# Optimization experiments

Hardware: AMD Instinct MI355X
Metric: run time of the kernel (lower is better)

The kernel has to match this reference:

```python
import jax, jax.numpy as jnp
import numpy as np

N_EMBD = 1024
N_HEAD = 16
B, T = 2, 2048
LN_EPS = 1e-5


def _linear_params(key, d_in, d_out):
    k1, k2 = jax.random.split(key)
    bound = 1.0 / np.sqrt(d_in)
    W = jax.random.uniform(k1, (d_in, d_out), jnp.float32, -bound, bound)
    b = jax.random.uniform(k2, (d_out,), jnp.float32, -bound, bound)
    return W, b


def setup_inputs() -> dict:
    key = jax.random.key(0)
    ks = jax.random.split(key, 8)
    x = jax.random.normal(ks[0], (B, T, N_EMBD), jnp.float32)
    Wq, bq = _linear_params(ks[1], N_EMBD, N_EMBD)
    Wk, bk = _linear_params(ks[2], N_EMBD, N_EMBD)
    Wv, bv = _linear_params(ks[3], N_EMBD, N_EMBD)
    Wo, bo = _linear_params(ks[4], N_EMBD, N_EMBD)
    W1, b1 = _linear_params(ks[5], N_EMBD, 4 * N_EMBD)
    W2, b2 = _linear_params(ks[6], 4 * N_EMBD, N_EMBD)
    ln1_g = jnp.ones((N_EMBD,), jnp.float32)
    ln1_b = jnp.zeros((N_EMBD,), jnp.float32)
    ln2_g = jnp.ones((N_EMBD,), jnp.float32)
    ln2_b = jnp.zeros((N_EMBD,), jnp.float32)
    return dict(x=x, Wq=Wq, bq=bq, Wk=Wk, bk=bk, Wv=Wv, bv=bv, Wo=Wo, bo=bo,
                W1=W1, b1=b1, W2=W2, b2=b2,
                ln1_g=ln1_g, ln1_b=ln1_b, ln2_g=ln2_g, ln2_b=ln2_b)


def _layernorm(x, g, b):
    mu = jnp.mean(x, axis=-1, keepdims=True)
    var = jnp.mean(jnp.square(x - mu), axis=-1, keepdims=True)
    return (x - mu) * jax.lax.rsqrt(var + LN_EPS) * g + b


def _attention(x, Wq, bq, Wk, bk, Wv, bv, Wo, bo):
    Bsz, Tlen, C = x.shape
    hd = C // N_HEAD
    q = (x @ Wq + bq).reshape(Bsz, Tlen, N_HEAD, hd)
    k = (x @ Wk + bk).reshape(Bsz, Tlen, N_HEAD, hd)
    v = (x @ Wv + bv).reshape(Bsz, Tlen, N_HEAD, hd)
    scale = 1.0 / np.sqrt(hd)
    # NOTE: the original module's mask buffer is all ones -> masked_fill is a
    # no-op, so attention is FULL (non-causal) despite the class name.
    att = jnp.einsum('bqhd,bkhd->bhqk', q, k) * scale
    att = jax.nn.softmax(att, axis=-1)
    y = jnp.einsum('bhqk,bkhd->bqhd', att, v).reshape(Bsz, Tlen, C)
    return y @ Wo + bo


def reference(x, Wq, bq, Wk, bk, Wv, bv, Wo, bo, W1, b1, W2, b2,
              ln1_g, ln1_b, ln2_g, ln2_b):
    x = x + _attention(_layernorm(x, ln1_g, ln1_b), Wq, bq, Wk, bk, Wv, bv, Wo, bo)
    h = _layernorm(x, ln2_g, ln2_b)
    h = jax.nn.gelu(h @ W1 + b1, approximate=False) @ W2 + b2
    return x + h
```

## Files before the change

### kernel.cpp

```cpp
#include <hip/hip_runtime.h>
#include <hip/hip_bf16.h>
#include <math.h>


typedef __bf16 bf16x8 __attribute__((ext_vector_type(8)));
typedef float f32x4 __attribute__((ext_vector_type(4)));

__device__ __forceinline__ unsigned short f2bf(float f) {
  union { float f; unsigned int u; } v; v.f = f;
  unsigned int u = v.u;
  unsigned int r = (u + 0x7fffu + ((u >> 16) & 1u)) >> 16;
  return (unsigned short)r;
}

__device__ __forceinline__ unsigned int fbits(float f) {
  union { float f; unsigned int u; } v; v.f = f;
  return v.u;
}

__device__ __forceinline__ bf16x8 ld_bf16x8(const unsigned short* p) {
  union { uint4 u; bf16x8 v; } x;
  x.u = *(const uint4*)p;
  return x.v;
}

__device__ __forceinline__ float fast_exp2(float x) {
#if __has_builtin(__builtin_amdgcn_exp2f)
  return __builtin_amdgcn_exp2f(x);
#else
  return exp2f(x);
#endif
}

__device__ __forceinline__ void barrier_lgkm_only() {
  asm volatile("s_waitcnt lgkmcnt(0)\n\ts_barrier" ::: "memory");
}

__device__ __forceinline__ void async_copy16(const void* g, void* l) {
  __builtin_amdgcn_global_load_lds(
      (const __attribute__((address_space(1))) void*)g,
      (__attribute__((address_space(3))) void*)l, 16, 0, 0);
}

__global__ __launch_bounds__(256) void transpose_cast_kernel(
    const float* __restrict__ W, unsigned short* __restrict__ Wt, int N, int K) {
  __shared__ unsigned short tile[32][33];
  const int n0 = blockIdx.x * 32, k0 = blockIdx.y * 32;
  const int t = threadIdx.x;
  const int r = t >> 3, cq = (t & 7) * 4;
  float4 v = *(const float4*)&W[(size_t)(k0 + r) * N + n0 + cq];
  tile[cq + 0][r] = f2bf(v.x);
  tile[cq + 1][r] = f2bf(v.y);
  tile[cq + 2][r] = f2bf(v.z);
  tile[cq + 3][r] = f2bf(v.w);
  __syncthreads();
  ushort4 o;
  o.x = tile[r][cq + 0];
  o.y = tile[r][cq + 1];
  o.z = tile[r][cq + 2];
  o.w = tile[r][cq + 3];
  *(ushort4*)&Wt[(size_t)(n0 + r) * K + k0 + cq] = o;
}

__global__ __launch_bounds__(256) void transpose_v_kernel(
    const unsigned short* __restrict__ V, unsigned short* __restrict__ Vt) {
  __shared__ unsigned short tile[32][36];
  const int kt = blockIdx.x * 32;
  const int d0 = blockIdx.y * 32;
  const int bh = blockIdx.z;
  const int bb = bh >> 4, h = bh & 15;
  const int t = threadIdx.x;
  const int r = t >> 3, c4 = (t & 7) * 4;
  ushort4 v = *(const ushort4*)&V[((size_t)bb * 2048 + kt + r) * 1024 + h * 64 + d0 + c4];
  tile[c4 + 0][r] = v.x;
  tile[c4 + 1][r] = v.y;
  tile[c4 + 2][r] = v.z;
  tile[c4 + 3][r] = v.w;
  __syncthreads();
  ushort4 o;
  o.x = tile[r][c4 + 0];
  o.y = tile[r][c4 + 1];
  o.z = tile[r][c4 + 2];
  o.w = tile[r][c4 + 3];
  *(ushort4*)&Vt[((size_t)bh * 64 + d0 + r) * 2048 + kt + c4] = o;
}

__global__ __launch_bounds__(256) void ln_kernel(
    const float* __restrict__ x, const float* __restrict__ g,
    const float* __restrict__ b, unsigned short* __restrict__ out) {
  const int row = blockIdx.x, t = threadIdx.x;
  const float4 v = ((const float4*)(x + (size_t)row * 1024))[t];
  float s = v.x + v.y + v.z + v.w;
  float s2 = v.x * v.x + v.y * v.y + v.z * v.z + v.w * v.w;
  for (int o = 32; o > 0; o >>= 1) {
    s += __shfl_xor(s, o, 64);
    s2 += __shfl_xor(s2, o, 64);
  }
  __shared__ float red[8];
  const int w = t >> 6;
  if ((t & 63) == 0) { red[w] = s; red[4 + w] = s2; }
  __syncthreads();
  s = red[0] + red[1] + red[2] + red[3];
  s2 = red[4] + red[5] + red[6] + red[7];
  const float mu = s * (1.f / 1024.f);
  const float var = s2 * (1.f / 1024.f) - mu * mu;
  const float rs = rsqrtf(var + 1e-5f);
  const float4 gg = ((const float4*)g)[t];
  const float4 bb = ((const float4*)b)[t];
  ushort4 o4;
  o4.x = f2bf((v.x - mu) * rs * gg.x + bb.x);
  o4.y = f2bf((v.y - mu) * rs * gg.y + bb.y);
  o4.z = f2bf((v.z - mu) * rs * gg.z + bb.z);
  o4.w = f2bf((v.w - mu) * rs * gg.w + bb.w);
  ((ushort4*)(out + (size_t)row * 1024))[t] = o4;
}

enum { MODE_QKV = 0, MODE_RES = 1, MODE_GELU = 2 };

#define QSCALE 0.18033688011112043f

template <int BM, int BN, int MODE>
__global__ __launch_bounds__(256) void gemm_kernel(
    const unsigned short* __restrict__ A, const unsigned short* __restrict__ Bt,
    const float* __restrict__ bias0, const float* __restrict__ bias1,
    const float* __restrict__ bias2, const float* __restrict__ residual,
    void* __restrict__ out0, void* __restrict__ out1, void* __restrict__ out2,
    int M, int N, int K) {
  constexpr int MI = BM / 32;
  constexpr int NI = BN / 32;
  __shared__ __align__(16) unsigned short As[2][2][BM * 32];
  __shared__ __align__(16) unsigned short Bs[2][2][BN * 32];
  const int t = threadIdx.x;

  const int NT = N / BN;
  const int NTX = NT >> 3;
  const int bid = blockIdx.x;
  const int xcd = bid & 7, local = bid >> 3;
  const int nt_ = xcd * NTX + local % NTX;
  const int mt = local / NTX;
  const int m0 = mt * BM, n0 = nt_ * BN;

  const int l = t & 63, w = t >> 6;
  const int wm = (w >> 1) * (BM / 2), wn = (w & 1) * (BN / 2);
  const int lr = l & 15, lq = l >> 4;

  f32x4 acc[MI][NI];
#pragma unroll
  for (int i = 0; i < MI; i++)
#pragma unroll
    for (int j = 0; j < NI; j++) {
      f32x4 z = {0.f, 0.f, 0.f, 0.f};
      acc[i][j] = z;
    }

  auto issue = [&](int k0, int p) {
#pragma unroll
    for (int h = 0; h < 2; h++)
#pragma unroll
      for (int s = 0; s < BM / 64; s++) {
        const int c = t + s * 256;
        const int row = c >> 2, k8 = (c & 3) * 8;
        async_copy16(&A[(size_t)(m0 + row) * K + k0 + h * 32 + k8],
                     &As[p][h][c * 8]);
      }
#pragma unroll
    for (int h = 0; h < 2; h++)
#pragma unroll
      for (int s = 0; s < BN / 64; s++) {
        const int c = t + s * 256;
        const int row = c >> 2, k8 = (c & 3) * 8;
        async_copy16(&Bt[(size_t)(n0 + row) * K + k0 + h * 32 + k8],
                     &Bs[p][h][c * 8]);
      }
  };

  issue(0, 0);
  int p = 0;
  for (int k0 = 0; k0 < K; k0 += 64) {
    __syncthreads();
    if (k0 + 64 < K) issue(k0 + 64, p ^ 1);
#pragma unroll
    for (int kk = 0; kk < 2; kk++) {
      bf16x8 af[MI], bf[NI];
#pragma unroll
      for (int mi = 0; mi < MI; mi++)
        af[mi] = ld_bf16x8(&As[p][kk][(wm + mi * 16 + lr) * 32 + lq * 8]);
#pragma unroll
      for (int ni = 0; ni < NI; ni++)
        bf[ni] = ld_bf16x8(&Bs[p][kk][(wn + ni * 16 + lr) * 32 + lq * 8]);
#pragma unroll
      for (int mi = 0; mi < MI; mi++)
#pragma unroll
        for (int ni = 0; ni < NI; ni++)
          acc[mi][ni] = __builtin_amdgcn_mfma_f32_16x16x32_bf16(
              af[mi], bf[ni], acc[mi][ni], 0, 0, 0);
    }
    p ^= 1;
  }

#pragma unroll
  for (int mi = 0; mi < MI; mi++) {
#pragma unroll
    for (int ni = 0; ni < NI; ni++) {
#pragma unroll
      for (int i = 0; i < 4; i++) {
        const int gm = m0 + wm + mi * 16 + lq * 4 + i;
        const int gn = n0 + wn + ni * 16 + lr;
        const float v = acc[mi][ni][i];
        if (MODE == MODE_QKV) {
          const int sel = gn >> 10, cn = gn & 1023;
          const float* bb = sel == 0 ? bias0 : (sel == 1 ? bias1 : bias2);
          unsigned short* dst =
              (unsigned short*)(sel == 0 ? out0 : (sel == 1 ? out1 : out2));
          float u = v + bb[cn];
          if (sel == 0) u *= QSCALE;
          dst[(size_t)gm * 1024 + cn] = f2bf(u);
        } else if (MODE == MODE_RES) {
          ((float*)out0)[(size_t)gm * N + gn] =
              v + bias0[gn] + residual[(size_t)gm * N + gn];
        } else {
          const float u = v + bias0[gn];
          const float ge = 0.5f * u * (1.f + erff(u * 0.70710678118654752f));
          ((unsigned short*)out0)[(size_t)gm * N + gn] = f2bf(ge);
        }
      }
    }
  }
}

__global__ __launch_bounds__(256) void attn_kernel(
    const unsigned short* __restrict__ Q, const unsigned short* __restrict__ Kt,
    const unsigned short* __restrict__ Vt, unsigned short* __restrict__ O) {
  __shared__ __align__(16) unsigned short QPs[128 * 72];
  __shared__ __align__(16) unsigned short Ks[2][64 * 72];
  __shared__ __align__(16) unsigned short Vs[2][64 * 72];
  const int id = blockIdx.x;
  const int xcd = id & 7, loc = id >> 3;
  const int bh = xcd * 4 + (loc >> 4);
  const int qt = loc & 15;
  const int bb = bh >> 4, h = bh & 15;
  const int t = threadIdx.x, l = t & 63, w = t >> 6;
  const int lr = l & 15, lq = l >> 4;
  const size_t rowBase = (size_t)bb * 2048;
  const int col0 = h * 64;

  const int sr = t >> 3;
  const int sc8 = (t & 7) * 8;

  uint4 kreg[2], vreg[2];
  auto issue_kv = [&](int kt) {
#pragma unroll
    for (int s = 0; s < 2; s++) {
      const int r = sr + s * 32;
      kreg[s] = *(const uint4*)&Kt[(rowBase + kt + r) * 1024 + col0 + sc8];
      vreg[s] = *(const uint4*)&Vt[((size_t)bh * 64 + r) * 2048 + kt + sc8];
    }
  };
  auto write_kv = [&](int p) {
#pragma unroll
    for (int s = 0; s < 2; s++) {
      const int r = sr + s * 32;
      *(uint4*)&Ks[p][r * 72 + sc8] = kreg[s];
      *(uint4*)&Vs[p][r * 72 + sc8] = vreg[s];
    }
  };

  issue_kv(0);

#pragma unroll
  for (int s = 0; s < 4; s++) {
    const int c = t + s * 256;
    const int r = c >> 3, c8 = (c & 7) * 8;
    *(uint4*)&QPs[r * 72 + c8] =
        *(const uint4*)&Q[(rowBase + qt * 128 + r) * 1024 + col0 + c8];
  }
  barrier_lgkm_only();
  bf16x8 qf[2][2];
#pragma unroll
  for (int s = 0; s < 2; s++)
#pragma unroll
    for (int kk = 0; kk < 2; kk++)
      qf[s][kk] = ld_bf16x8(&QPs[(w * 32 + s * 16 + lr) * 72 + kk * 32 + lq * 8]);

  write_kv(0);
  issue_kv(64);
  barrier_lgkm_only();

  f32x4 oacc[2][4];
#pragma unroll
  for (int s = 0; s < 2; s++)
#pragma unroll
    for (int nt = 0; nt < 4; nt++) {
      f32x4 z = {0.f, 0.f, 0.f, 0.f};
      oacc[s][nt] = z;
    }
  float lp[2] = {0.f, 0.f};

  int p = 0;
  for (int kt = 0; kt < 2048; kt += 64) {
    if (kt + 64 < 2048) {
      write_kv(p ^ 1);
      if (kt + 128 < 2048) issue_kv(kt + 128);
    }

    f32x4 st[2][4];
#pragma unroll
    for (int s = 0; s < 2; s++)
#pragma unroll
      for (int nt = 0; nt < 4; nt++) {
        f32x4 z = {0.f, 0.f, 0.f, 0.f};
        st[s][nt] = z;
      }
#pragma unroll
    for (int nt = 0; nt < 4; nt++) {
      bf16x8 kf0 = ld_bf16x8(&Ks[p][(nt * 16 + lr) * 72 + 0 * 32 + lq * 8]);
      bf16x8 kf1 = ld_bf16x8(&Ks[p][(nt * 16 + lr) * 72 + 1 * 32 + lq * 8]);
      __builtin_amdgcn_s_setprio(1);
      st[0][nt] = __builtin_amdgcn_mfma_f32_16x16x32_bf16(kf0, qf[0][0], st[0][nt], 0, 0, 0);
      st[1][nt] = __builtin_amdgcn_mfma_f32_16x16x32_bf16(kf0, qf[1][0], st[1][nt], 0, 0, 0);
      st[0][nt] = __builtin_amdgcn_mfma_f32_16x16x32_bf16(kf1, qf[0][1], st[0][nt], 0, 0, 0);
      st[1][nt] = __builtin_amdgcn_mfma_f32_16x16x32_bf16(kf1, qf[1][1], st[1][nt], 0, 0, 0);
      __builtin_amdgcn_s_setprio(0);
    }

    bf16x8 vf[2][4];
#pragma unroll
    for (int kb = 0; kb < 2; kb++)
#pragma unroll
      for (int nt = 0; nt < 4; nt++)
        vf[kb][nt] = ld_bf16x8(&Vs[p][(nt * 16 + lr) * 72 + kb * 32 + lq * 8]);

#pragma unroll
    for (int s = 0; s < 2; s++) {
      float rsum = 0.f;
#pragma unroll
      for (int nt = 0; nt < 4; nt++)
#pragma unroll
        for (int i = 0; i < 4; i++) {
          const float pv = fast_exp2(st[s][nt][i]);
          st[s][nt][i] = pv;
          rsum += pv;
        }
      lp[s] += rsum;
    }

#pragma unroll
    for (int s = 0; s < 2; s++)
#pragma unroll
      for (int nt = 0; nt < 4; nt++) {
        uint2 pk;
        pk.x = __builtin_amdgcn_perm(fbits(st[s][nt][1]), fbits(st[s][nt][0]), 0x07060302u);
        pk.y = __builtin_amdgcn_perm(fbits(st[s][nt][3]), fbits(st[s][nt][2]), 0x07060302u);
        *(uint2*)&QPs[(w * 32 + s * 16 + lr) * 72 + nt * 16 + lq * 4] = pk;
      }

#pragma unroll
    for (int kb = 0; kb < 2; kb++) {
      bf16x8 pf0 = ld_bf16x8(&QPs[(w * 32 + lr) * 72 + kb * 32 + lq * 8]);
      bf16x8 pf1 = ld_bf16x8(&QPs[(w * 32 + 16 + lr) * 72 + kb * 32 + lq * 8]);
      __builtin_amdgcn_s_setprio(1);
#pragma unroll
      for (int nt = 0; nt < 4; nt++) {
        oacc[0][nt] = __builtin_amdgcn_mfma_f32_16x16x32_bf16(pf0, vf[kb][nt], oacc[0][nt], 0, 0, 0);
        oacc[1][nt] = __builtin_amdgcn_mfma_f32_16x16x32_bf16(pf1, vf[kb][nt], oacc[1][nt], 0, 0, 0);
      }
      __builtin_amdgcn_s_setprio(0);
    }

    if (kt + 64 < 2048) barrier_lgkm_only();
    p ^= 1;
  }

#pragma unroll
  for (int s = 0; s < 2; s++) {
    float li = lp[s];
    li += __shfl_xor(li, 16, 64);
    li += __shfl_xor(li, 32, 64);
    const float inv = 1.f / li;
#pragma unroll
    for (int nt = 0; nt < 4; nt++)
#pragma unroll
      for (int i = 0; i < 4; i++) {
        const size_t orow = rowBase + qt * 128 + w * 32 + s * 16 + lq * 4 + i;
        const int ocol = col0 + nt * 16 + lr;
        O[orow * 1024 + ocol] = f2bf(oacc[s][nt][i] * inv);
      }
  }
}

extern "C" void kernel_launch(void* const* d_in, const int* in_sizes, int n_in,
                              void* d_out, int out_size, void* d_ws, size_t ws_size,
                              hipStream_t stream) {
  const float* x    = (const float*)d_in[0];
  const float* Wq   = (const float*)d_in[1];
  const float* bq   = (const float*)d_in[2];
  const float* Wk   = (const float*)d_in[3];
  const float* bk   = (const float*)d_in[4];
  const float* Wv   = (const float*)d_in[5];
  const float* bv   = (const float*)d_in[6];
  const float* Wo   = (const float*)d_in[7];
  const float* bo   = (const float*)d_in[8];
  const float* W1   = (const float*)d_in[9];
  const float* b1   = (const float*)d_in[10];
  const float* W2   = (const float*)d_in[11];
  const float* b2   = (const float*)d_in[12];
  const float* ln1g = (const float*)d_in[13];
  const float* ln1b = (const float*)d_in[14];
  const float* ln2g = (const float*)d_in[15];
  const float* ln2b = (const float*)d_in[16];

  char* ws = (char*)d_ws;
  const size_t MB = 1024ull * 1024ull;
  unsigned short* WqT = (unsigned short*)(ws + 0 * MB);
  unsigned short* WkT = (unsigned short*)(ws + 2 * MB);
  unsigned short* WvT = (unsigned short*)(ws + 4 * MB);
  unsigned short* WoT = (unsigned short*)(ws + 6 * MB);
  unsigned short* W1T = (unsigned short*)(ws + 8 * MB);
  unsigned short* W2T = (unsigned short*)(ws + 16 * MB);
  unsigned short* xn  = (unsigned short*)(ws + 24 * MB);
  unsigned short* Qb  = (unsigned short*)(ws + 32 * MB);
  unsigned short* Kb  = (unsigned short*)(ws + 40 * MB);
  unsigned short* Vb  = (unsigned short*)(ws + 48 * MB);
  unsigned short* Ob  = (unsigned short*)(ws + 56 * MB);
  float*          x1  = (float*)(ws + 64 * MB);
  unsigned short* h2  = (unsigned short*)(ws + 80 * MB);
  unsigned short* VtG = (unsigned short*)(ws + 24 * MB);
  unsigned short* Hb  = (unsigned short*)(ws + 24 * MB);

  const dim3 blk(256);

  transpose_cast_kernel<<<dim3(32, 32), blk, 0, stream>>>(Wq, WqT, 1024, 1024);
  transpose_cast_kernel<<<dim3(32, 32), blk, 0, stream>>>(Wk, WkT, 1024, 1024);
  transpose_cast_kernel<<<dim3(32, 32), blk, 0, stream>>>(Wv, WvT, 1024, 1024);
  transpose_cast_kernel<<<dim3(32, 32), blk, 0, stream>>>(Wo, WoT, 1024, 1024);
  transpose_cast_kernel<<<dim3(128, 32), blk, 0, stream>>>(W1, W1T, 4096, 1024);
  transpose_cast_kernel<<<dim3(32, 128), blk, 0, stream>>>(W2, W2T, 1024, 4096);

  ln_kernel<<<4096, blk, 0, stream>>>(x, ln1g, ln1b, xn);

  gemm_kernel<128, 128, MODE_QKV><<<dim3(24 * 32), blk, 0, stream>>>(
      xn, WqT, bq, bk, bv, nullptr, Qb, Kb, Vb, 4096, 3072, 1024);

  transpose_v_kernel<<<dim3(64, 2, 32), blk, 0, stream>>>(Vb, VtG);

  attn_kernel<<<dim3(512), blk, 0, stream>>>(Qb, Kb, VtG, Ob);

  gemm_kernel<64, 128, MODE_RES><<<dim3(8 * 64), blk, 0, stream>>>(
      Ob, WoT, bo, nullptr, nullptr, x, x1, nullptr, nullptr, 4096, 1024, 1024);

  ln_kernel<<<4096, blk, 0, stream>>>(x1, ln2g, ln2b, h2);

  gemm_kernel<128, 128, MODE_GELU><<<dim3(32 * 32), blk, 0, stream>>>(
      h2, W1T, b1, nullptr, nullptr, nullptr, Hb, nullptr, nullptr, 4096, 4096, 1024);

  gemm_kernel<64, 128, MODE_RES><<<dim3(8 * 64), blk, 0, stream>>>(
      Hb, W2T, b2, nullptr, nullptr, x1, (float*)d_out, nullptr, nullptr, 4096, 1024, 4096);
}
```

Baseline: 418.1 us.

## Load Q/K/V fragments directly from global memory into registers in attention

Removes the shared-memory staging of K and V tiles and the Q tile in the attention kernel. Each wave now loads its MFMA fragments straight from global memory (L2/L1), prefetching the next K tile into registers during softmax. Per-iteration block barriers are dropped, and only the per-wave P buffer stays in LDS. The trade-off is that each of the 4 waves fetches the same K/V data, roughly quadrupling global/L1 traffic, in exchange for fewer LDS round-trips and no synchronisation.

```diff
diff --git a/kernel.cpp b/kernel.cpp
--- a/kernel.cpp
+++ b/kernel.cpp
@@ -30,10 +30,6 @@
 #else
   return exp2f(x);
 #endif
-}
-
-__device__ __forceinline__ void barrier_lgkm_only() {
-  asm volatile("s_waitcnt lgkmcnt(0)\n\ts_barrier" ::: "memory");
 }
 
 __device__ __forceinline__ void async_copy16(const void* g, void* l) {
@@ -231,9 +227,7 @@
 __global__ __launch_bounds__(256) void attn_kernel(
     const unsigned short* __restrict__ Q, const unsigned short* __restrict__ Kt,
     const unsigned short* __restrict__ Vt, unsigned short* __restrict__ O) {
-  __shared__ __align__(16) unsigned short QPs[128 * 72];
-  __shared__ __align__(16) unsigned short Ks[2][64 * 72];
-  __shared__ __align__(16) unsigned short Vs[2][64 * 72];
+  __shared__ __align__(16) unsigned short Ps[128 * 72];
   const int id = blockIdx.x;
   const int xcd = id & 7, loc = id >> 3;
   const int bh = xcd * 4 + (loc >> 4);
@@ -244,47 +238,22 @@
   const size_t rowBase = (size_t)bb * 2048;
   const int col0 = h * 64;
 
-  const int sr = t >> 3;
-  const int sc8 = (t & 7) * 8;
-
-  uint4 kreg[2], vreg[2];
-  auto issue_kv = [&](int kt) {
-#pragma unroll
-    for (int s = 0; s < 2; s++) {
-      const int r = sr + s * 32;
-      kreg[s] = *(const uint4*)&Kt[(rowBase + kt + r) * 1024 + col0 + sc8];
-      vreg[s] = *(const uint4*)&Vt[((size_t)bh * 64 + r) * 2048 + kt + sc8];
-    }
-  };
-  auto write_kv = [&](int p) {
-#pragma unroll
-    for (int s = 0; s < 2; s++) {
-      const int r = sr + s * 32;
-      *(uint4*)&Ks[p][r * 72 + sc8] = kreg[s];
-      *(uint4*)&Vs[p][r * 72 + sc8] = vreg[s];
-    }
-  };
-
-  issue_kv(0);
-
-#pragma unroll
-  for (int s = 0; s < 4; s++) {
-    const int c = t + s * 256;
-    const int r = c >> 3, c8 = (c & 7) * 8;
-    *(uint4*)&QPs[r * 72 + c8] =
-        *(const uint4*)&Q[(rowBase + qt * 128 + r) * 1024 + col0 + c8];
-  }
-  barrier_lgkm_only();
   bf16x8 qf[2][2];
 #pragma unroll
   for (int s = 0; s < 2; s++)
 #pragma unroll
     for (int kk = 0; kk < 2; kk++)
-      qf[s][kk] = ld_bf16x8(&QPs[(w * 32 + s * 16 + lr) * 72 + kk * 32 + lq * 8]);
-
-  write_kv(0);
-  issue_kv(64);
-  barrier_lgkm_only();
+      qf[s][kk] = ld_bf16x8(
+          &Q[(rowBase + qt * 128 + w * 32 + s * 16 + lr) * 1024 + col0 +
+             kk * 32 + lq * 8]);
+
+  bf16x8 kf[2][4];
+#pragma unroll
+  for (int nt = 0; nt < 4; nt++)
+#pragma unroll
+    for (int kk = 0; kk < 2; kk++)
+      kf[kk][nt] = ld_bf16x8(
+          &Kt[(rowBase + nt * 16 + lr) * 1024 + col0 + kk * 32 + lq * 8]);
 
   f32x4 oacc[2][4];
 #pragma unroll
@@ -296,12 +265,15 @@
     }
   float lp[2] = {0.f, 0.f};
 
-  int p = 0;
   for (int kt = 0; kt < 2048; kt += 64) {
-    if (kt + 64 < 2048) {
-      write_kv(p ^ 1);
-      if (kt + 128 < 2048) issue_kv(kt + 128);
-    }
+    bf16x8 vf[2][4];
+#pragma unroll
+    for (int nt = 0; nt < 4; nt++)
+#pragma unroll
+      for (int kb = 0; kb < 2; kb++)
+        vf[kb][nt] = ld_bf16x8(
+            &Vt[((size_t)bh * 64 + nt * 16 + lr) * 2048 + kt + kb * 32 +
+                lq * 8]);
 
     f32x4 st[2][4];
 #pragma unroll
@@ -313,22 +285,22 @@
       }
 #pragma unroll
     for (int nt = 0; nt < 4; nt++) {
-      bf16x8 kf0 = ld_bf16x8(&Ks[p][(nt * 16 + lr) * 72 + 0 * 32 + lq * 8]);
-      bf16x8 kf1 = ld_bf16x8(&Ks[p][(nt * 16 + lr) * 72 + 1 * 32 + lq * 8]);
       __builtin_amdgcn_s_setprio(1);
-      st[0][nt] = __builtin_amdgcn_mfma_f32_16x16x32_bf16(kf0, qf[0][0], st[0][nt], 0, 0, 0);
-      st[1][nt] = __builtin_amdgcn_mfma_f32_16x16x32_bf16(kf0, qf[1][0], st[1][nt], 0, 0, 0);
-      st[0][nt] = __builtin_amdgcn_mfma_f32_16x16x32_bf16(kf1, qf[0][1], st[0][nt], 0, 0, 0);
-      st[1][nt] = __builtin_amdgcn_mfma_f32_16x16x32_bf16(kf1, qf[1][1], st[1][nt], 0, 0, 0);
+      st[0][nt] = __builtin_amdgcn_mfma_f32_16x16x32_bf16(kf[0][nt], qf[0][0], st[0][nt], 0, 0, 0);
+      st[1][nt] = __builtin_amdgcn_mfma_f32_16x16x32_bf16(kf[0][nt], qf[1][0], st[1][nt], 0, 0, 0);
+      st[0][nt] = __builtin_amdgcn_mfma_f32_16x16x32_bf16(kf[1][nt], qf[0][1], st[0][nt], 0, 0, 0);
+      st[1][nt] = __builtin_amdgcn_mfma_f32_16x16x32_bf16(kf[1][nt], qf[1][1], st[1][nt], 0, 0, 0);
       __builtin_amdgcn_s_setprio(0);
     }
 
-    bf16x8 vf[2][4];
-#pragma unroll
-    for (int kb = 0; kb < 2; kb++)
-#pragma unroll
-      for (int nt = 0; nt < 4; nt++)
-        vf[kb][nt] = ld_bf16x8(&Vs[p][(nt * 16 + lr) * 72 + kb * 32 + lq * 8]);
+    const int ktn = (kt + 64) & 2047;
+#pragma unroll
+    for (int nt = 0; nt < 4; nt++)
+#pragma unroll
+      for (int kk = 0; kk < 2; kk++)
+        kf[kk][nt] = ld_bf16x8(
+            &Kt[(rowBase + ktn + nt * 16 + lr) * 1024 + col0 + kk * 32 +
+                lq * 8]);
 
 #pragma unroll
     for (int s = 0; s < 2; s++) {
@@ -351,13 +323,13 @@
         uint2 pk;
         pk.x = __builtin_amdgcn_perm(fbits(st[s][nt][1]), fbits(st[s][nt][0]), 0x07060302u);
         pk.y = __builtin_amdgcn_perm(fbits(st[s][nt][3]), fbits(st[s][nt][2]), 0x07060302u);
-        *(uint2*)&QPs[(w * 32 + s * 16 + lr) * 72 + nt * 16 + lq * 4] = pk;
+        *(uint2*)&Ps[(w * 32 + s * 16 + lr) * 72 + nt * 16 + lq * 4] = pk;
       }
 
 #pragma unroll
     for (int kb = 0; kb < 2; kb++) {
-      bf16x8 pf0 = ld_bf16x8(&QPs[(w * 32 + lr) * 72 + kb * 32 + lq * 8]);
-      bf16x8 pf1 = ld_bf16x8(&QPs[(w * 32 + 16 + lr) * 72 + kb * 32 + lq * 8]);
+      bf16x8 pf0 = ld_bf16x8(&Ps[(w * 32 + lr) * 72 + kb * 32 + lq * 8]);
+      bf16x8 pf1 = ld_bf16x8(&Ps[(w * 32 + 16 + lr) * 72 + kb * 32 + lq * 8]);
       __builtin_amdgcn_s_setprio(1);
 #pragma unroll
       for (int nt = 0; nt < 4; nt++) {
@@ -366,9 +338,6 @@
       }
       __builtin_amdgcn_s_setprio(0);
     }
-
-    if (kt + 64 < 2048) barrier_lgkm_only();
-    p ^= 1;
   }
 
 #pragma unroll
```

After: 448.2 us. 1.07x slower.
